# Performance work log

Measured on AMD Instinct MI355X. Metric: run time of the kernel, lower is better.

## Reference

```python
import jax, jax.numpy as jnp
import numpy as np

B, S, HID = 1, 2048, 2048
H, D, R = 16, 256, 64          # heads, head_dim, qk_rope_head_dim
NOPE = D - R
QL, OR, G = 1024, 512, 4       # q_lora_rank, o_lora_rank, o_groups
HPG = H // G
EPS = 1e-6
SCALE = D ** -0.5
STD = 0.02


def setup_inputs() -> dict:
    key = jax.random.key(0)
    ks = jax.random.split(key, 9)
    return {
        "x": jax.random.normal(ks[0], (B, S, HID), jnp.float32),
        "freqs": jax.random.uniform(ks[1], (B, S, R // 2), jnp.float32) * 6.2831853,
        "wq_a": jax.random.normal(ks[2], (QL, HID), jnp.float32) * STD,
        "q_norm_w": jnp.ones((QL,), jnp.float32),
        "wq_b": jax.random.normal(ks[3], (H * D, QL), jnp.float32) * STD,
        "wkv": jax.random.normal(ks[4], (D, HID), jnp.float32) * STD,
        "kv_norm_w": jnp.ones((D,), jnp.float32),
        "wo_a_w": jax.random.normal(ks[5], (G * OR, HPG * D), jnp.float32) * STD,
        "wo_b": jax.random.normal(ks[6], (HID, G * OR), jnp.float32) * STD,
        "attn_sink": jnp.zeros((H,), jnp.float32),
    }


def _rms(x, w):
    return x * jax.lax.rsqrt(jnp.mean(jnp.square(x), -1, keepdims=True) + EPS) * w


def _rot(t, cos, sin, conj=False):
    # t: [..., R]; cos/sin broadcastable to [..., R//2]
    tr = t.reshape(*t.shape[:-1], R // 2, 2)
    x1, x2 = tr[..., 0], tr[..., 1]
    if conj:
        sin = -sin
    out = jnp.stack([x1 * cos - x2 * sin, x1 * sin + x2 * cos], axis=-1)
    return out.reshape(t.shape)


def reference(x, freqs, wq_a, q_norm_w, wq_b, wkv, kv_norm_w, wo_a_w, wo_b, attn_sink):
    cos = jnp.cos(freqs)  # [B,S,R/2]
    sin = jnp.sin(freqs)

    # Q path: LoRA down -> RMSNorm -> up, then per-head RMS rescale (no weight)
    q = _rms(x @ wq_a.T, q_norm_w) @ wq_b.T          # [B,S,H*D]
    q = q.reshape(B, S, H, D)
    q = q * jax.lax.rsqrt(jnp.mean(jnp.square(q), -1, keepdims=True) + EPS)
    q_nope, q_pe = q[..., :NOPE], q[..., NOPE:]

    # shared latent K=V
    kv = _rms(x @ wkv.T, kv_norm_w)                  # [B,S,D]
    kv_nope, kv_pe = kv[..., :NOPE], kv[..., NOPE:]

    # partial RoPE
    q_pe = _rot(q_pe, cos[:, :, None, :], sin[:, :, None, :])
    kv_pe = _rot(kv_pe, cos, sin)

    q = jnp.concatenate([q_nope, q_pe], -1)          # [B,S,H,D]
    kv = jnp.concatenate([kv_nope, kv_pe], -1)       # [B,S,D] shared across heads

    # attention with causal mask + per-head sink column
    scores = jnp.einsum("bshd,btd->bhst", q, kv) * SCALE   # [B,H,S,S]
    mask = jnp.tril(jnp.ones((S, S), bool))
    scores = jnp.where(mask, scores, -jnp.inf)
    sink = jnp.broadcast_to(attn_sink[None, :, None, None], (B, H, S, 1))
    probs = jax.nn.softmax(jnp.concatenate([scores, sink], -1), axis=-1)[..., :-1]
    o = jnp.einsum("bhst,btd->bshd", probs, kv)      # [B,S,H,D]

    # un-rotate the rope part of the output (multiply by conj(freqs_cis))
    o_nope, o_pe = o[..., :NOPE], o[..., NOPE:]
    o_pe = _rot(o_pe, cos[:, :, None, :], sin[:, :, None, :], conj=True)
    o = jnp.concatenate([o_nope, o_pe], -1)

    # grouped (block-diagonal) output LoRA, then up-projection
    o_g = o.reshape(B, S, G, HPG * D)
    w = wo_a_w.reshape(G, OR, HPG * D)
    o_r = jnp.einsum("bsgd,grd->bsgr", o_g, w).reshape(B, S, G * OR)
    return o_r @ wo_b.T                              # [B,S,HID]
```

## Files before the change

### kernel.cpp

```cpp
#include <hip/hip_runtime.h>
#include <hip/hip_bf16.h>

#define S_LEN 2048
#define HID 2048
#define NH 16
#define HD 256
#define NROT 64
#define NOPE 192
#define QL 1024
#define OR_ 512
#define NG 4
#define HPG 4
#define EPS 1e-6f
#define SCALE 0.0625f

typedef __bf16 bf16x8 __attribute__((ext_vector_type(8)));
typedef short s16x8 __attribute__((ext_vector_type(8)));
typedef float f32x4 __attribute__((ext_vector_type(4)));

#define MFMA(a, b, c) __builtin_amdgcn_mfma_f32_16x16x32_bf16( \
    __builtin_bit_cast(bf16x8, a), __builtin_bit_cast(bf16x8, b), c, 0, 0, 0)

__device__ __forceinline__ unsigned short f2bf(float x) {
  unsigned int u = __builtin_bit_cast(unsigned int, x);
  u += 0x7FFFu + ((u >> 16) & 1u);
  return (unsigned short)(u >> 16);
}
__device__ __forceinline__ float bf2f(unsigned short b) {
  unsigned int u = ((unsigned int)b) << 16;
  return __builtin_bit_cast(float, u);
}

#define GLD_LDS16(gp, lp) __builtin_amdgcn_global_load_lds( \
    (__attribute__((address_space(1))) void*)(gp), \
    (__attribute__((address_space(3))) void*)(lp), 16, 0, 0)

__global__ __launch_bounds__(256) void f32_to_bf16(const float* __restrict__ in,
                                                   unsigned short* __restrict__ out, int n4) {
  int i = blockIdx.x * 256 + threadIdx.x;
  if (i < n4) {
    float4 v = ((const float4*)in)[i];
    ushort4 o;
    o.x = f2bf(v.x); o.y = f2bf(v.y); o.z = f2bf(v.z); o.w = f2bf(v.w);
    ((ushort4*)out)[i] = o;
  }
}

__global__ __launch_bounds__(256) void conv5(
    const float* __restrict__ x, const float* __restrict__ wqa,
    const float* __restrict__ wqb, const float* __restrict__ wkv,
    const float* __restrict__ woa,
    unsigned short* __restrict__ xo, unsigned short* __restrict__ wqao,
    unsigned short* __restrict__ wqbo, unsigned short* __restrict__ wkvo,
    unsigned short* __restrict__ woao) {
  int i = blockIdx.x * 256 + threadIdx.x;
  const float* src; unsigned short* dst; int off;
  if (i < 1048576)      { src = x;   dst = xo;   off = i; }
  else if (i < 1572864) { src = wqa; dst = wqao; off = i - 1048576; }
  else if (i < 2621440) { src = wqb; dst = wqbo; off = i - 1572864; }
  else if (i < 2752512) { src = wkv; dst = wkvo; off = i - 2621440; }
  else                  { src = woa; dst = woao; off = i - 2752512; }
  float4 v = ((const float4*)src)[off];
  ushort4 o;
  o.x = f2bf(v.x); o.y = f2bf(v.y); o.z = f2bf(v.z); o.w = f2bf(v.w);
  ((ushort4*)dst)[off] = o;
}

template <int BN>
__global__ __launch_bounds__(256, 2) void gemm_bf16(
    const unsigned short* __restrict__ A, const unsigned short* __restrict__ B,
    void* __restrict__ Cv, int K, int lda, int ldb, int ldc,
    long aoffz, long boffz, long coffz, int store_bf) {
  constexpr int NF = BN / 32;
  __shared__ __align__(16) unsigned short As[128 * 128];
  __shared__ __align__(16) unsigned short Bs[BN * 128];
  A += (size_t)blockIdx.z * aoffz;
  B += (size_t)blockIdx.z * boffz;
  const int tid = threadIdx.x;
  const int wave = tid >> 6, lane = tid & 63;
  const int col = lane & 15, grp = lane >> 4;
  const int wm = wave >> 1, wn = wave & 1;
  const int m0 = blockIdx.y * 128, n0 = blockIdx.x * BN;

  f32x4 acc[4][NF];
#pragma unroll
  for (int i = 0; i < 4; ++i)
#pragma unroll
    for (int j = 0; j < NF; ++j) acc[i][j] = (f32x4){0.f, 0.f, 0.f, 0.f};

  for (int k0 = 0; k0 < K; k0 += 128) {
#pragma unroll
    for (int u = 0; u < 8; ++u) {
      int lin = u * 256 + tid;
      int r = lin >> 4, c = lin & 15;
      GLD_LDS16(A + (size_t)(m0 + r) * lda + k0 + (c ^ (r & 7)) * 8, &As[lin * 8]);
    }
#pragma unroll
    for (int u = 0; u < BN / 16; ++u) {
      int lin = u * 256 + tid;
      int r = lin >> 4, c = lin & 15;
      GLD_LDS16(B + (size_t)(n0 + r) * ldb + k0 + (c ^ (r & 7)) * 8, &Bs[lin * 8]);
    }
    __syncthreads();
#pragma unroll
    for (int kk = 0; kk < 128; kk += 32) {
      s16x8 a[4], b[NF];
#pragma unroll
      for (int i = 0; i < 4; ++i) {
        int row = wm * 64 + i * 16 + col;
        int g = (kk >> 3) + grp;
        a[i] = *(const s16x8*)&As[row * 128 + ((g ^ (row & 7)) * 8)];
      }
#pragma unroll
      for (int j = 0; j < NF; ++j) {
        int row = wn * (BN / 2) + j * 16 + col;
        int g = (kk >> 3) + grp;
        b[j] = *(const s16x8*)&Bs[row * 128 + ((g ^ (row & 7)) * 8)];
      }
#pragma unroll
      for (int i = 0; i < 4; ++i)
#pragma unroll
        for (int j = 0; j < NF; ++j)
          acc[i][j] = MFMA(a[i], b[j], acc[i][j]);
    }
    __syncthreads();
  }

  if (store_bf) {
    unsigned short* C = (unsigned short*)Cv + (size_t)blockIdx.z * coffz;
#pragma unroll
    for (int i = 0; i < 4; ++i)
#pragma unroll
      for (int j = 0; j < NF; ++j)
#pragma unroll
        for (int r = 0; r < 4; ++r)
          C[(size_t)(m0 + wm * 64 + i * 16 + grp * 4 + r) * ldc +
            n0 + wn * (BN / 2) + j * 16 + col] = f2bf(acc[i][j][r]);
  } else {
    float* C = (float*)Cv + (size_t)blockIdx.z * coffz;
#pragma unroll
    for (int i = 0; i < 4; ++i)
#pragma unroll
      for (int j = 0; j < NF; ++j)
#pragma unroll
        for (int r = 0; r < 4; ++r)
          C[(size_t)(m0 + wm * 64 + i * 16 + grp * 4 + r) * ldc +
            n0 + wn * (BN / 2) + j * 16 + col] = acc[i][j][r];
  }
}

__global__ __launch_bounds__(256) void rms_combine2(const float* __restrict__ p,
                                                    unsigned short* __restrict__ out,
                                                    const float* __restrict__ w) {
  int row = blockIdx.x;
  const float* r0 = p + (size_t)row * QL;
  const float* r1 = r0 + 2097152;
  __shared__ float buf[QL];
  __shared__ float red[256];
  float s = 0.f;
  for (int i = threadIdx.x; i < QL; i += 256) {
    float v = r0[i] + r1[i];
    buf[i] = v;
    s += v * v;
  }
  red[threadIdx.x] = s;
  __syncthreads();
  for (int off = 128; off > 0; off >>= 1) {
    if (threadIdx.x < off) red[threadIdx.x] += red[threadIdx.x + off];
    __syncthreads();
  }
  float r = rsqrtf(red[0] / (float)QL + EPS);
  for (int i = threadIdx.x; i < QL; i += 256)
    out[(size_t)row * QL + i] = f2bf(buf[i] * r * w[i]);
}

__global__ __launch_bounds__(256) void kv_combine8(const float* __restrict__ p,
                                                   const float* __restrict__ w,
                                                   const float* __restrict__ freqs,
                                                   unsigned short* __restrict__ kv,
                                                   unsigned short* __restrict__ kvT) {
  int s = blockIdx.x;
  int d = threadIdx.x;
  const float* b = p + (size_t)s * HD + d;
  float v = 0.f;
#pragma unroll
  for (int z = 0; z < 8; ++z) v += b[(size_t)z * 524288];
  __shared__ float red[256];
  __shared__ float sm[256];
  red[d] = v * v;
  __syncthreads();
  for (int off = 128; off > 0; off >>= 1) {
    if (d < off) red[d] += red[d + off];
    __syncthreads();
  }
  float r = rsqrtf(red[0] / 256.0f + EPS);
  float nv = v * r * w[d];
  sm[d] = nv;
  __syncthreads();
  float outv = nv;
  if (d >= NOPE) {
    int j = (d - NOPE) >> 1;
    float f = freqs[(size_t)s * (NROT / 2) + j];
    float c = cosf(f), si = sinf(f);
    float x1 = sm[NOPE + 2 * j], x2 = sm[NOPE + 2 * j + 1];
    outv = ((d & 1) == 0) ? (x1 * c - x2 * si) : (x1 * si + x2 * c);
  }
  unsigned short ov = f2bf(outv);
  kv[(size_t)s * HD + d] = ov;
  kvT[(size_t)(s & ~63) * HD + d * 64 + (s & 63)] = ov;
}

__global__ __launch_bounds__(256, 2) void attn_mfma(
    const unsigned short* __restrict__ qbf,
    const unsigned short* __restrict__ kvbf,
    const unsigned short* __restrict__ kvT,
    const float* __restrict__ sink,
    const float* __restrict__ freqs,
    unsigned short* __restrict__ ob) {
  __shared__ __align__(16) unsigned short kv_s[64 * 264];
  __shared__ __align__(16) unsigned short p_s[64 * 72];
  __shared__ float alpha_s[64];
  __shared__ float inv_s[64];

  const int tid = threadIdx.x;
  const int wave = tid >> 6, lane = tid & 63;
  const int col = lane & 15, grp = lane >> 4;
  const int lin = blockIdx.y * gridDim.x + blockIdx.x;
  const int half = lin >> 8, li = lin & 255;
  const int tr = li & 31;
  const int h = (half == 0) ? (li >> 5) : 8 + (li >> 5);
  const int q0 = ((half == 0) ? (31 - tr) : tr) * 64;
  const int qrow = q0 + wave * 16;

  const unsigned short* qbase =
      qbf + (size_t)(qrow + col) * (NH * HD) + (size_t)h * HD + grp * 8;
#define QDECL(ko, nam) s16x8 nam = *(const s16x8*)(qbase + (ko) * 32);
  QDECL(0, qf0) QDECL(1, qf1) QDECL(2, qf2) QDECL(3, qf3)
  QDECL(4, qf4) QDECL(5, qf5) QDECL(6, qf6) QDECL(7, qf7)

  {
    float sq = 0.f;
#define QSQ(qf) { _Pragma("unroll") \
    for (int j = 0; j < 8; ++j) { float v = bf2f((unsigned short)qf[j]); sq += v * v; } }
    QSQ(qf0) QSQ(qf1) QSQ(qf2) QSQ(qf3) QSQ(qf4) QSQ(qf5) QSQ(qf6) QSQ(qf7)
    sq += __shfl_xor(sq, 16);
    sq += __shfl_xor(sq, 32);
    const float qr_ = rsqrtf(sq * (1.0f / 256.0f) + EPS);
#define QSC(qf) { _Pragma("unroll") \
    for (int j = 0; j < 8; ++j) qf[j] = (short)f2bf(bf2f((unsigned short)qf[j]) * qr_); }
    QSC(qf0) QSC(qf1) QSC(qf2) QSC(qf3) QSC(qf4) QSC(qf5)
    const float* fb = freqs + (size_t)(qrow + col) * (NROT / 2);
#define QSR(qf, jb) { _Pragma("unroll") \
    for (int u = 0; u < 4; ++u) { \
      float f = fb[(jb) + grp * 4 + u]; \
      float c = cosf(f), s = sinf(f); \
      float x1 = bf2f((unsigned short)qf[2 * u]) * qr_; \
      float x2 = bf2f((unsigned short)qf[2 * u + 1]) * qr_; \
      qf[2 * u]     = (short)f2bf(x1 * c - x2 * s); \
      qf[2 * u + 1] = (short)f2bf(x1 * s + x2 * c); } }
    QSR(qf6, 0) QSR(qf7, 16)
  }

  const f32x4 z4 = (f32x4){0.f, 0.f, 0.f, 0.f};
  float m0r = -1e30f, m1r = -1e30f, m2r = -1e30f, m3r = -1e30f;
  float lp0 = 0.f, lp1 = 0.f, lp2 = 0.f, lp3 = 0.f;

#define FOR16(M) M(0,0,o00) M(0,1,o01) M(0,2,o02) M(0,3,o03) \
                 M(1,0,o10) M(1,1,o11) M(1,2,o12) M(1,3,o13) \
                 M(2,0,o20) M(2,1,o21) M(2,2,o22) M(2,3,o23) \
                 M(3,0,o30) M(3,1,o31) M(3,2,o32) M(3,3,o33)
#define DECLO(i, j, onam) f32x4 onam = z4;
  FOR16(DECLO)

  const int tS = tid >> 5, ddS = (tid & 31) * 8;

  {
    const unsigned short* sb = kvbf + (size_t)tS * HD + ddS;
#pragma unroll
    for (int k = 0; k < 8; ++k)
      *(s16x8*)&kv_s[(tS + 8 * k) * 264 + ddS] = *(const s16x8*)(sb + (size_t)(8 * k) * HD);
  }

  const int nch = q0 / 64 + 1;
  for (int ch = 0; ch < nch; ++ch) {
    const int t0 = ch * 64;
    __syncthreads();

    const bool havest = (ch + 1 < nch);
    s16x8 st0 = {}, st1 = {}, st2 = {}, st3 = {}, st4 = {}, st5 = {}, st6 = {}, st7 = {};
    if (havest) {
      const unsigned short* sb = kvbf + (size_t)(t0 + 64 + tS) * HD + ddS;
      st0 = *(const s16x8*)(sb);
      st1 = *(const s16x8*)(sb + 8 * HD);
      st2 = *(const s16x8*)(sb + 16 * HD);
      st3 = *(const s16x8*)(sb + 24 * HD);
      st4 = *(const s16x8*)(sb + 32 * HD);
      st5 = *(const s16x8*)(sb + 40 * HD);
      st6 = *(const s16x8*)(sb + 48 * HD);
      st7 = *(const s16x8*)(sb + 56 * HD);
    }
    const unsigned short* vb = kvT + (size_t)t0 * HD + (size_t)(wave * 64 + col) * 64 + grp * 8;
    s16x8 vf00 = *(const s16x8*)(vb);
    s16x8 vf01 = *(const s16x8*)(vb + 32);
    s16x8 vf10 = *(const s16x8*)(vb + 16 * 64);
    s16x8 vf11 = *(const s16x8*)(vb + 16 * 64 + 32);
    s16x8 vf20 = *(const s16x8*)(vb + 32 * 64);
    s16x8 vf21 = *(const s16x8*)(vb + 32 * 64 + 32);
    s16x8 vf30 = *(const s16x8*)(vb + 48 * 64);
    s16x8 vf31 = *(const s16x8*)(vb + 48 * 64 + 32);

    f32x4 sA0 = z4, sA1 = z4, sA2 = z4, sA3 = z4;
    __builtin_amdgcn_s_setprio(1);
#define QKS(ko, qf) { \
      s16x8 b0 = *(const s16x8*)&kv_s[col * 264 + (ko) * 32 + grp * 8]; \
      s16x8 b1 = *(const s16x8*)&kv_s[(16 + col) * 264 + (ko) * 32 + grp * 8]; \
      s16x8 b2 = *(const s16x8*)&kv_s[(32 + col) * 264 + (ko) * 32 + grp * 8]; \
      s16x8 b3 = *(const s16x8*)&kv_s[(48 + col) * 264 + (ko) * 32 + grp * 8]; \
      sA0 = MFMA(qf, b0, sA0); sA1 = MFMA(qf, b1, sA1); \
      sA2 = MFMA(qf, b2, sA2); sA3 = MFMA(qf, b3, sA3); }
    QKS(0, qf0) QKS(1, qf1) QKS(2, qf2) QKS(3, qf3)
    QKS(4, qf4) QKS(5, qf5) QKS(6, qf6) QKS(7, qf7)
    __builtin_amdgcn_s_setprio(0);

#define MASKR(r) { int sg = qrow + grp * 4 + (r); \
    sA0[r] = (t0 + col <= sg)      ? sA0[r] * SCALE : -1e30f; \
    sA1[r] = (t0 + 16 + col <= sg) ? sA1[r] * SCALE : -1e30f; \
    sA2[r] = (t0 + 32 + col <= sg) ? sA2[r] * SCALE : -1e30f; \
    sA3[r] = (t0 + 48 + col <= sg) ? sA3[r] * SCALE : -1e30f; }
    MASKR(0) MASKR(1) MASKR(2) MASKR(3)

    float a0, a1, a2, a3;
#define MAXR(r, mr, ar) { \
    float v = fmaxf(fmaxf(sA0[r], sA1[r]), fmaxf(sA2[r], sA3[r])); \
    v = fmaxf(v, __shfl_xor(v, 1)); v = fmaxf(v, __shfl_xor(v, 2)); \
    v = fmaxf(v, __shfl_xor(v, 4)); v = fmaxf(v, __shfl_xor(v, 8)); \
    float mn = fmaxf(mr, v); ar = __expf(mr - mn); mr = mn; }
    MAXR(0, m0r, a0) MAXR(1, m1r, a1) MAXR(2, m2r, a2) MAXR(3, m3r, a3)

#define PROW(r, mr, lpr, ar) { \
    float p0 = __expf(sA0[r] - mr); float p1 = __expf(sA1[r] - mr); \
    float p2 = __expf(sA2[r] - mr); float p3 = __expf(sA3[r] - mr); \
    lpr = lpr * ar + (p0 + p1) + (p2 + p3); \
    int prow = (wave * 16 + grp * 4 + (r)) * 72; \
    p_s[prow + col] = f2bf(p0);      p_s[prow + 16 + col] = f2bf(p1); \
    p_s[prow + 32 + col] = f2bf(p2); p_s[prow + 48 + col] = f2bf(p3); }
    PROW(0, m0r, lp0, a0) PROW(1, m1r, lp1, a1) PROW(2, m2r, lp2, a2) PROW(3, m3r, lp3, a3)

    if (col == 0) {
      alpha_s[wave * 16 + grp * 4 + 0] = a0;
      alpha_s[wave * 16 + grp * 4 + 1] = a1;
      alpha_s[wave * 16 + grp * 4 + 2] = a2;
      alpha_s[wave * 16 + grp * 4 + 3] = a3;
    }
    __syncthreads();

    if (havest) {
      *(s16x8*)&kv_s[tS * 264 + ddS]        = st0;
      *(s16x8*)&kv_s[(tS + 8) * 264 + ddS]  = st1;
      *(s16x8*)&kv_s[(tS + 16) * 264 + ddS] = st2;
      *(s16x8*)&kv_s[(tS + 24) * 264 + ddS] = st3;
      *(s16x8*)&kv_s[(tS + 32) * 264 + ddS] = st4;
      *(s16x8*)&kv_s[(tS + 40) * 264 + ddS] = st5;
      *(s16x8*)&kv_s[(tS + 48) * 264 + ddS] = st6;
      *(s16x8*)&kv_s[(tS + 56) * 264 + ddS] = st7;
    }

#define RESC(i) { f32x4 av = (f32x4){alpha_s[(i)*16 + grp*4 + 0], alpha_s[(i)*16 + grp*4 + 1], \
                                     alpha_s[(i)*16 + grp*4 + 2], alpha_s[(i)*16 + grp*4 + 3]}; \
    o##i##0 *= av; o##i##1 *= av; o##i##2 *= av; o##i##3 *= av; }
    RESC(0) RESC(1) RESC(2) RESC(3)

    s16x8 pf00 = *(const s16x8*)&p_s[(0 * 16 + col) * 72 + grp * 8];
    s16x8 pf01 = *(const s16x8*)&p_s[(0 * 16 + col) * 72 + 32 + grp * 8];
    s16x8 pf10 = *(const s16x8*)&p_s[(1 * 16 + col) * 72 + grp * 8];
    s16x8 pf11 = *(const s16x8*)&p_s[(1 * 16 + col) * 72 + 32 + grp * 8];
    s16x8 pf20 = *(const s16x8*)&p_s[(2 * 16 + col) * 72 + grp * 8];
    s16x8 pf21 = *(const s16x8*)&p_s[(2 * 16 + col) * 72 + 32 + grp * 8];
    s16x8 pf30 = *(const s16x8*)&p_s[(3 * 16 + col) * 72 + grp * 8];
    s16x8 pf31 = *(const s16x8*)&p_s[(3 * 16 + col) * 72 + 32 + grp * 8];
    __builtin_amdgcn_s_setprio(1);
#define PVJ(j) { \
      o0##j = MFMA(pf00, vf##j##0, o0##j); o0##j = MFMA(pf01, vf##j##1, o0##j); \
      o1##j = MFMA(pf10, vf##j##0, o1##j); o1##j = MFMA(pf11, vf##j##1, o1##j); \
      o2##j = MFMA(pf20, vf##j##0, o2##j); o2##j = MFMA(pf21, vf##j##1, o2##j); \
      o3##j = MFMA(pf30, vf##j##0, o3##j); o3##j = MFMA(pf31, vf##j##1, o3##j); }
    PVJ(0) PVJ(1) PVJ(2) PVJ(3)
    __builtin_amdgcn_s_setprio(0);
  }

  const float sk = sink[h];
  {
#define LRED(lpr) { lpr += __shfl_xor(lpr, 1); lpr += __shfl_xor(lpr, 2); \
                    lpr += __shfl_xor(lpr, 4); lpr += __shfl_xor(lpr, 8); }
    LRED(lp0) LRED(lp1) LRED(lp2) LRED(lp3)
    float i0 = 1.f / (lp0 + __expf(sk - m0r));
    float i1 = 1.f / (lp1 + __expf(sk - m1r));
    float i2 = 1.f / (lp2 + __expf(sk - m2r));
    float i3 = 1.f / (lp3 + __expf(sk - m3r));
    if (col == 0) {
      inv_s[wave * 16 + grp * 4 + 0] = i0;
      inv_s[wave * 16 + grp * 4 + 1] = i1;
      inv_s[wave * 16 + grp * 4 + 2] = i2;
      inv_s[wave * 16 + grp * 4 + 3] = i3;
    }
  }
  __syncthreads();

#define EPIJ(i, j, onam, ivv) { \
    float v0 = onam[0] * ivv[0]; float v1 = onam[1] * ivv[1]; \
    float v2 = onam[2] * ivv[2]; float v3 = onam[3] * ivv[3]; \
    if (wave == 3) { \
      int jr = ((j) * 16 + col) >> 1; \
      float f0 = freqs[(size_t)(q0 + (i) * 16 + grp * 4 + 0) * 32 + jr]; \
      float f1 = freqs[(size_t)(q0 + (i) * 16 + grp * 4 + 1) * 32 + jr]; \
      float f2 = freqs[(size_t)(q0 + (i) * 16 + grp * 4 + 2) * 32 + jr]; \
      float f3 = freqs[(size_t)(q0 + (i) * 16 + grp * 4 + 3) * 32 + jr]; \
      float p0 = __shfl_xor(v0, 1), p1 = __shfl_xor(v1, 1); \
      float p2 = __shfl_xor(v2, 1), p3 = __shfl_xor(v3, 1); \
      v0 = (col & 1) ? (v0 * cosf(f0) - p0 * sinf(f0)) : (v0 * cosf(f0) + p0 * sinf(f0)); \
      v1 = (col & 1) ? (v1 * cosf(f1) - p1 * sinf(f1)) : (v1 * cosf(f1) + p1 * sinf(f1)); \
      v2 = (col & 1) ? (v2 * cosf(f2) - p2 * sinf(f2)) : (v2 * cosf(f2) + p2 * sinf(f2)); \
      v3 = (col & 1) ? (v3 * cosf(f3) - p3 * sinf(f3)) : (v3 * cosf(f3) + p3 * sinf(f3)); \
    } \
    size_t obase = (size_t)(q0 + (i) * 16 + grp * 4) * (NH * HD) + (size_t)h * HD + \
                   wave * 64 + (j) * 16 + col; \
    ob[obase] = f2bf(v0); ob[obase + (NH * HD)] = f2bf(v1); \
    ob[obase + 2 * (NH * HD)] = f2bf(v2); ob[obase + 3 * (NH * HD)] = f2bf(v3); }
#define EPII(i) { \
    f32x4 ivv = (f32x4){inv_s[(i)*16 + grp*4 + 0], inv_s[(i)*16 + grp*4 + 1], \
                        inv_s[(i)*16 + grp*4 + 2], inv_s[(i)*16 + grp*4 + 3]}; \
    EPIJ(i, 0, o##i##0, ivv) EPIJ(i, 1, o##i##1, ivv) \
    EPIJ(i, 2, o##i##2, ivv) EPIJ(i, 3, o##i##3, ivv) }
  EPII(0) EPII(1) EPII(2) EPII(3)
}

extern "C" void kernel_launch(void* const* d_in, const int* in_sizes, int n_in,
                              void* d_out, int out_size, void* d_ws, size_t ws_size,
                              hipStream_t stream) {
  const float* x         = (const float*)d_in[0];
  const float* freqs     = (const float*)d_in[1];
  const float* wq_a      = (const float*)d_in[2];
  const float* q_norm_w  = (const float*)d_in[3];
  const float* wq_b      = (const float*)d_in[4];
  const float* wkv       = (const float*)d_in[5];
  const float* kv_norm_w = (const float*)d_in[6];
  const float* wo_a_w    = (const float*)d_in[7];
  const float* wo_b      = (const float*)d_in[8];
  const float* sink      = (const float*)d_in[9];
  float* out = (float*)d_out;

  char* ws = (char*)d_ws;
  const size_t MB = 1024 * 1024;
  unsigned short* qa_bf   = (unsigned short*)(ws + 0 * MB);
  float*          qa_p    = (float*)(ws + 4 * MB);
  unsigned short* q_bf    = (unsigned short*)(ws + 4 * MB);
  unsigned short* orb_bf  = (unsigned short*)(ws + 4 * MB);
  unsigned short* wob_bf  = (unsigned short*)(ws + 12 * MB);
  unsigned short* o_bf    = (unsigned short*)(ws + 20 * MB);
  unsigned short* x_bf    = (unsigned short*)(ws + 20 * MB);
  float*          kv_p    = (float*)(ws + 28 * MB);
  unsigned short* wqa_bf  = (unsigned short*)(ws + 36 * MB);
  unsigned short* wqb_bf  = (unsigned short*)(ws + 40 * MB);
  unsigned short* wkv_bf  = (unsigned short*)(ws + 48 * MB);
  unsigned short* woa_bf  = (unsigned short*)(ws + 49 * MB);
  unsigned short* kv_bf   = (unsigned short*)(ws + 53 * MB);
  unsigned short* kvT_bf  = (unsigned short*)(ws + 54 * MB);

  dim3 blk(256);

  conv5<<<dim3(12800), blk, 0, stream>>>(x, wq_a, wq_b, wkv, wo_a_w,
                                         x_bf, wqa_bf, wqb_bf, wkv_bf, woa_bf);

  gemm_bf16<64><<<dim3(QL / 64, S_LEN / 128, 2), blk, 0, stream>>>(
      x_bf, wqa_bf, qa_p, HID / 2, HID, HID, QL,
      (long)(HID / 2), (long)(HID / 2), (long)S_LEN * QL, 0);
  rms_combine2<<<dim3(S_LEN), blk, 0, stream>>>(qa_p, qa_bf, q_norm_w);
  gemm_bf16<128><<<dim3(NH * HD / 128, S_LEN / 128, 1), blk, 0, stream>>>(
      qa_bf, wqb_bf, q_bf, QL, QL, QL, NH * HD, 0, 0, 0, 1);
  gemm_bf16<64><<<dim3(HD / 64, S_LEN / 128, 8), blk, 0, stream>>>(
      x_bf, wkv_bf, kv_p, HID / 8, HID, HID, HD,
      (long)(HID / 8), (long)(HID / 8), (long)S_LEN * HD, 0);
  kv_combine8<<<dim3(S_LEN), blk, 0, stream>>>(kv_p, kv_norm_w, freqs, kv_bf, kvT_bf);
  attn_mfma<<<dim3(S_LEN / 64, NH), blk, 0, stream>>>(q_bf, kv_bf, kvT_bf, sink, freqs, o_bf);
  f32_to_bf16<<<dim3(4096), blk, 0, stream>>>(wo_b, wob_bf, 4 * 1024 * 1024 / 4);
  gemm_bf16<64><<<dim3(OR_ / 64, S_LEN / 128, NG), blk, 0, stream>>>(
      o_bf, woa_bf, orb_bf, HPG * HD, NH * HD, HPG * HD, NG * OR_,
      (long)(HPG * HD), (long)OR_ * (HPG * HD), (long)OR_, 1);
  gemm_bf16<64><<<dim3(HID / 64, S_LEN / 128, 1), blk, 0, stream>>>(
      orb_bf, wob_bf, out, NG * OR_, NG * OR_, NG * OR_, HID, 0, 0, 0, 0);
}
```

Baseline: 357.6 us.

## Fuse Q-down and KV projection GEMMs into one split-K launch

Replaces the separate split-K GEMMs for x@wq_a and x@wkv with a single kernel whose z index selects either a Q-down slice (K=1024, two splits) or a KV slice (K=512, four splits). Blocks beyond the KV column range exit early. KV split-K drops from 8 to 4 partials, so kv_combine now sums four buffers. The goal is to cut one launch and fill the GPU better by running both projections concurrently, at the cost of some idle early-exit blocks and fewer KV splits.

```diff
diff --git a/kernel.cpp b/kernel.cpp
--- a/kernel.cpp
+++ b/kernel.cpp
@@ -149,6 +149,87 @@
   }
 }
 
+__global__ __launch_bounds__(256, 2) void gemm_qakv(
+    const unsigned short* __restrict__ xb, const unsigned short* __restrict__ wqa,
+    const unsigned short* __restrict__ wkv, float* __restrict__ qa_p,
+    float* __restrict__ kv_p) {
+  constexpr int BN = 64, NF = 2;
+  const unsigned short* A;
+  const unsigned short* B;
+  float* C;
+  int K, ldc;
+  const int z = blockIdx.z;
+  if (z < 2) {
+    A = xb + z * 1024; B = wqa + z * 1024;
+    C = qa_p + (size_t)z * S_LEN * QL; K = 1024; ldc = QL;
+  } else {
+    if (blockIdx.x >= HD / 64) return;
+    int zz = z - 2;
+    A = xb + zz * 512; B = wkv + zz * 512;
+    C = kv_p + (size_t)zz * S_LEN * HD; K = 512; ldc = HD;
+  }
+  __shared__ __align__(16) unsigned short As[128 * 128];
+  __shared__ __align__(16) unsigned short Bs[BN * 128];
+  const int tid = threadIdx.x;
+  const int wave = tid >> 6, lane = tid & 63;
+  const int col = lane & 15, grp = lane >> 4;
+  const int wm = wave >> 1, wn = wave & 1;
+  const int m0 = blockIdx.y * 128, n0 = blockIdx.x * BN;
+
+  f32x4 acc[4][NF];
+#pragma unroll
+  for (int i = 0; i < 4; ++i)
+#pragma unroll
+    for (int j = 0; j < NF; ++j) acc[i][j] = (f32x4){0.f, 0.f, 0.f, 0.f};
+
+  for (int k0 = 0; k0 < K; k0 += 128) {
+#pragma unroll
+    for (int u = 0; u < 8; ++u) {
+      int lin = u * 256 + tid;
+      int r = lin >> 4, c = lin & 15;
+      GLD_LDS16(A + (size_t)(m0 + r) * HID + k0 + (c ^ (r & 7)) * 8, &As[lin * 8]);
+    }
+#pragma unroll
+    for (int u = 0; u < BN / 16; ++u) {
+      int lin = u * 256 + tid;
+      int r = lin >> 4, c = lin & 15;
+      GLD_LDS16(B + (size_t)(n0 + r) * HID + k0 + (c ^ (r & 7)) * 8, &Bs[lin * 8]);
+    }
+    __syncthreads();
+#pragma unroll
+    for (int kk = 0; kk < 128; kk += 32) {
+      s16x8 a[4], b[NF];
+#pragma unroll
+      for (int i = 0; i < 4; ++i) {
+        int row = wm * 64 + i * 16 + col;
+        int g = (kk >> 3) + grp;
+        a[i] = *(const s16x8*)&As[row * 128 + ((g ^ (row & 7)) * 8)];
+      }
+#pragma unroll
+      for (int j = 0; j < NF; ++j) {
+        int row = wn * (BN / 2) + j * 16 + col;
+        int g = (kk >> 3) + grp;
+        b[j] = *(const s16x8*)&Bs[row * 128 + ((g ^ (row & 7)) * 8)];
+      }
+#pragma unroll
+      for (int i = 0; i < 4; ++i)
+#pragma unroll
+        for (int j = 0; j < NF; ++j)
+          acc[i][j] = MFMA(a[i], b[j], acc[i][j]);
+    }
+    __syncthreads();
+  }
+
+#pragma unroll
+  for (int i = 0; i < 4; ++i)
+#pragma unroll
+    for (int j = 0; j < NF; ++j)
+#pragma unroll
+      for (int r = 0; r < 4; ++r)
+        C[(size_t)(m0 + wm * 64 + i * 16 + grp * 4 + r) * ldc +
+          n0 + wn * (BN / 2) + j * 16 + col] = acc[i][j][r];
+}
+
 __global__ __launch_bounds__(256) void rms_combine2(const float* __restrict__ p,
                                                     unsigned short* __restrict__ out,
                                                     const float* __restrict__ w) {
@@ -174,7 +255,7 @@
     out[(size_t)row * QL + i] = f2bf(buf[i] * r * w[i]);
 }
 
-__global__ __launch_bounds__(256) void kv_combine8(const float* __restrict__ p,
+__global__ __launch_bounds__(256) void kv_combine4(const float* __restrict__ p,
                                                    const float* __restrict__ w,
                                                    const float* __restrict__ freqs,
                                                    unsigned short* __restrict__ kv,
@@ -184,7 +265,7 @@
   const float* b = p + (size_t)s * HD + d;
   float v = 0.f;
 #pragma unroll
-  for (int z = 0; z < 8; ++z) v += b[(size_t)z * 524288];
+  for (int z = 0; z < 4; ++z) v += b[(size_t)z * 524288];
   __shared__ float red[256];
   __shared__ float sm[256];
   red[d] = v * v;
@@ -471,16 +552,12 @@
   conv5<<<dim3(12800), blk, 0, stream>>>(x, wq_a, wq_b, wkv, wo_a_w,
                                          x_bf, wqa_bf, wqb_bf, wkv_bf, woa_bf);
 
-  gemm_bf16<64><<<dim3(QL / 64, S_LEN / 128, 2), blk, 0, stream>>>(
-      x_bf, wqa_bf, qa_p, HID / 2, HID, HID, QL,
-      (long)(HID / 2), (long)(HID / 2), (long)S_LEN * QL, 0);
+  gemm_qakv<<<dim3(QL / 64, S_LEN / 128, 6), blk, 0, stream>>>(
+      x_bf, wqa_bf, wkv_bf, qa_p, kv_p);
   rms_combine2<<<dim3(S_LEN), blk, 0, stream>>>(qa_p, qa_bf, q_norm_w);
+  kv_combine4<<<dim3(S_LEN), blk, 0, stream>>>(kv_p, kv_norm_w, freqs, kv_bf, kvT_bf);
   gemm_bf16<128><<<dim3(NH * HD / 128, S_LEN / 128, 1), blk, 0, stream>>>(
       qa_bf, wqb_bf, q_bf, QL, QL, QL, NH * HD, 0, 0, 0, 1);
-  gemm_bf16<64><<<dim3(HD / 64, S_LEN / 128, 8), blk, 0, stream>>>(
-      x_bf, wkv_bf, kv_p, HID / 8, HID, HID, HD,
-      (long)(HID / 8), (long)(HID / 8), (long)S_LEN * HD, 0);
-  kv_combine8<<<dim3(S_LEN), blk, 0, stream>>>(kv_p, kv_norm_w, freqs, kv_bf, kvT_bf);
   attn_mfma<<<dim3(S_LEN / 64, NH), blk, 0, stream>>>(q_bf, kv_bf, kvT_bf, sink, freqs, o_bf);
   f32_to_bf16<<<dim3(4096), blk, 0, stream>>>(wo_b, wob_bf, 4 * 1024 * 1024 / 4);
   gemm_bf16<64><<<dim3(OR_ / 64, S_LEN / 128, NG), blk, 0, stream>>>(
```

Measured after the change: 355.4 us. No clear change (-0.6%).
